# Performance work log

Measured on AMD Instinct MI355X. Metric: run time of the kernel, lower is better.

Reference implementation:

```python
import jax, jax.numpy as jnp
import numpy as np

N_NODES = 100000
N_EDGES = 1600000
D_IN = 128
D_OUT = 128
EPS = 1e-5


def setup_inputs() -> dict:
    key = jax.random.key(0)
    k1, k2, k3, k4, k5 = jax.random.split(key, 5)
    x = jax.random.normal(k1, (N_NODES, D_IN), dtype=jnp.float32)
    row = jax.random.randint(k2, (N_EDGES,), 0, N_NODES, dtype=jnp.int64)
    col = jax.random.randint(k3, (N_EDGES,), 0, N_NODES, dtype=jnp.int64)
    adj_vals = jax.random.uniform(k4, (N_EDGES,), dtype=jnp.float32)
    # Xavier-uniform init for weight, zeros for bias (as in the torch module)
    limit = float(np.sqrt(6.0 / (D_IN + D_OUT)))
    weight = jax.random.uniform(k5, (D_IN, D_OUT), minval=-limit, maxval=limit, dtype=jnp.float32)
    bias = jnp.zeros((D_OUT,), dtype=jnp.float32)
    return {"x": x, "row": row, "col": col, "adj_vals": adj_vals, "weight": weight, "bias": bias}


def reference(x, row, col, adj_vals, weight, bias):
    # degree = row-sum of sparse adj
    degree = jax.ops.segment_sum(adj_vals, row, num_segments=N_NODES)
    degree = jnp.where(degree == 0, EPS, degree)
    d_inv_sqrt = (degree + EPS) ** -0.5  # [N]
    # edge-wise symmetric normalization: D^-1/2 A D^-1/2
    edge_w = d_inv_sqrt[row] * adj_vals * d_inv_sqrt[col]  # [E]
    # SpMM: gather neighbor features, scale, scatter-add to destination rows
    msgs = edge_w[:, None] * x[col]  # [E, D_IN]
    agg = jax.ops.segment_sum(msgs, row, num_segments=N_NODES)  # [N, D_IN]
    return agg @ weight + bias
```

## Files before the change

### kernel.cpp

```cpp
#include <hip/hip_runtime.h>

#define NN 100000
#define NE 1600000
#define D  128
#define EPS 1e-5f

#define NBKT   782
#define NEB    391
#define EPB_H  4096
#define GRID_G 782
#define NSCAN  (NBKT*NEB)
#define GRID2  299
#define CAP    2560

#define OFF_HCNT 0x0000000ULL
#define OFF_PART 0x0140000ULL
#define OFF_BASE 0x0142000ULL
#define OFF_DINV 0x0150000ULL
#define OFF_GREC 0x0200000ULL
#define OFF_YB   0x0F00000ULL

typedef short short8 __attribute__((ext_vector_type(8)));
typedef float f32x4 __attribute__((ext_vector_type(4)));

static __device__ __forceinline__ unsigned f2bf(float f) {
    unsigned u = __float_as_uint(f);
    return (u + 0x7fffu + ((u >> 16) & 1u)) >> 16;
}

__global__ void k0h(const int* __restrict__ row, unsigned* __restrict__ hcnt) {
    __shared__ unsigned h[NBKT];
    int t = threadIdx.x, b = blockIdx.x;
    for (int i = t; i < NBKT; i += 256) h[i] = 0;
    __syncthreads();
    int ebeg = b * EPB_H;
    for (int i = t; i < EPB_H; i += 256) {
        int e = ebeg + i;
        if (e < NE) atomicAdd(&h[((unsigned)row[e]) >> 7], 1u);
    }
    __syncthreads();
    for (int i = t; i < NBKT; i += 256) hcnt[i * NEB + b] = h[i];
}

__global__ void k2a(const unsigned* __restrict__ hcnt, unsigned* __restrict__ part) {
    __shared__ unsigned s[256];
    int t = threadIdx.x;
    int gi = blockIdx.x * 1024 + t * 4;
    unsigned v = 0;
    #pragma unroll
    for (int j = 0; j < 4; ++j) if (gi + j < NSCAN) v += hcnt[gi + j];
    s[t] = v;
    __syncthreads();
    for (int d = 128; d > 0; d >>= 1) {
        if (t < d) s[t] += s[t + d];
        __syncthreads();
    }
    if (t == 0) part[blockIdx.x] = s[0];
}

__launch_bounds__(512)
__global__ void k2b(const unsigned* __restrict__ part, unsigned* __restrict__ base) {
    __shared__ unsigned s[512];
    int t = threadIdx.x;
    unsigned v = (t < GRID2) ? part[t] : 0;
    s[t] = v;
    __syncthreads();
    for (int d = 1; d < 512; d <<= 1) {
        unsigned u = (t >= d) ? s[t - d] : 0;
        __syncthreads();
        s[t] += u;
        __syncthreads();
    }
    if (t < GRID2) base[t] = s[t] - v;
}

__global__ void k2c(unsigned* __restrict__ hcnt, const unsigned* __restrict__ base) {
    __shared__ unsigned s[256];
    int t = threadIdx.x;
    int gi = blockIdx.x * 1024 + t * 4;
    unsigned v[4], tot = 0;
    #pragma unroll
    for (int j = 0; j < 4; ++j) {
        v[j] = (gi + j < NSCAN) ? hcnt[gi + j] : 0;
        tot += v[j];
    }
    s[t] = tot;
    __syncthreads();
    for (int d = 1; d < 256; d <<= 1) {
        unsigned u = (t >= d) ? s[t - d] : 0;
        __syncthreads();
        s[t] += u;
        __syncthreads();
    }
    unsigned run = base[blockIdx.x] + s[t] - tot;
    #pragma unroll
    for (int j = 0; j < 4; ++j) {
        if (gi + j < NSCAN) { hcnt[gi + j] = run; run += v[j]; }
    }
}

__launch_bounds__(256)
__global__ void k3(const int* __restrict__ row, const int* __restrict__ col,
                   const float* __restrict__ adj, const unsigned* __restrict__ hcnt,
                   unsigned long long* __restrict__ grec) {
    __shared__ unsigned cur[NBKT];
    int t = threadIdx.x, b = blockIdx.x;
    for (int i = t; i < NBKT; i += 256) cur[i] = hcnt[i * NEB + b];
    __syncthreads();
    int ebeg = b * EPB_H;
    for (int i = t; i < EPB_H; i += 256) {
        int e = ebeg + i;
        if (e >= NE) continue;
        unsigned r = (unsigned)row[e];
        unsigned aq = (unsigned)rintf(adj[e] * 32767.0f);
        unsigned lo = (unsigned)col[e] | (aq << 17);
        unsigned dst = atomicAdd(&cur[r >> 7], 1u);
        grec[dst] = (unsigned long long)lo | ((unsigned long long)(r & 127u) << 32);
    }
}

__global__ void k4a(const unsigned* __restrict__ hcnt, const unsigned long long* __restrict__ grec,
                    float* __restrict__ dinv) {
    __shared__ unsigned s[128];
    int t = threadIdx.x, b = blockIdx.x;
    if (t < 128) s[t] = 0;
    __syncthreads();
    unsigned beg = hcnt[b * NEB];
    unsigned end = (b == NBKT - 1) ? NE : hcnt[(b + 1) * NEB];
    for (unsigned p = beg + t; p < end; p += 256) {
        unsigned long long rec = grec[p];
        atomicAdd(&s[(unsigned)(rec >> 32) & 127u], ((unsigned)rec >> 17) & 0x7FFFu);
    }
    __syncthreads();
    if (t < 128) {
        int r = b * 128 + t;
        if (r < NN) {
            float d = (float)s[t] * (1.0f / 32767.0f);
            d = (d == 0.0f) ? EPS : d;
            dinv[r] = rsqrtf(d + EPS);
        }
    }
}

__launch_bounds__(256, 2)
__global__ void k1g(const float* __restrict__ x, const float* __restrict__ w,
                    const float* __restrict__ dinv, unsigned short* __restrict__ yb) {
    __shared__ unsigned short sx[128 * 128];
    __shared__ unsigned short sw[128 * 128];
    int tid = threadIdx.x;
    int base = blockIdx.x * 128;

    #pragma unroll
    for (int i = 0; i < 8; ++i) {
        int task = i * 256 + tid;
        int n = task & 127, ko = task >> 7;
        const float* wp = w + (size_t)(ko * 8) * D + n;
        uint4 pk;
        pk.x = f2bf(wp[0])     | (f2bf(wp[D])     << 16);
        pk.y = f2bf(wp[2 * D]) | (f2bf(wp[3 * D]) << 16);
        pk.z = f2bf(wp[4 * D]) | (f2bf(wp[5 * D]) << 16);
        pk.w = f2bf(wp[6 * D]) | (f2bf(wp[7 * D]) << 16);
        int idx = (n * 128 + ko * 8) ^ ((n & 7) << 3);
        *(uint4*)(&sw[idx]) = pk;
    }
    #pragma unroll
    for (int i = 0; i < 8; ++i) {
        int task = i * 256 + tid;
        int ko = task & 15, r = task >> 4;
        int gr = base + r;
        float4 f0 = make_float4(0.f, 0.f, 0.f, 0.f), f1 = f0;
        if (gr < NN) {
            const float* xp = x + (size_t)gr * D + ko * 8;
            f0 = *(const float4*)xp;
            f1 = *(const float4*)(xp + 4);
        }
        uint4 pk;
        pk.x = f2bf(f0.x) | (f2bf(f0.y) << 16);
        pk.y = f2bf(f0.z) | (f2bf(f0.w) << 16);
        pk.z = f2bf(f1.x) | (f2bf(f1.y) << 16);
        pk.w = f2bf(f1.z) | (f2bf(f1.w) << 16);
        int idx = (r * 128 + ko * 8) ^ ((r & 7) << 3);
        *(uint4*)(&sx[idx]) = pk;
    }
    __syncthreads();

    int wv = tid >> 6, l = tid & 63;
    int lr = l & 15, g = l >> 4;

    f32x4 acc[2][8];
    #pragma unroll
    for (int ti = 0; ti < 2; ++ti)
        #pragma unroll
        for (int tj = 0; tj < 8; ++tj)
            acc[ti][tj] = (f32x4){0.f, 0.f, 0.f, 0.f};

    #pragma unroll
    for (int kc = 0; kc < 4; ++kc) {
        int kb = kc * 32 + g * 8;
        short8 a[2], b[8];
        #pragma unroll
        for (int ti = 0; ti < 2; ++ti) {
            int r0 = wv * 32 + ti * 16 + lr;
            a[ti] = *(const short8*)(&sx[(r0 * 128 + kb) ^ ((r0 & 7) << 3)]);
        }
        #pragma unroll
        for (int tj = 0; tj < 8; ++tj) {
            int n0 = tj * 16 + lr;
            b[tj] = *(const short8*)(&sw[(n0 * 128 + kb) ^ ((n0 & 7) << 3)]);
        }
        #pragma unroll
        for (int ti = 0; ti < 2; ++ti)
            #pragma unroll
            for (int tj = 0; tj < 8; ++tj)
                acc[ti][tj] = __builtin_amdgcn_mfma_f32_16x16x32_bf16(
                    a[ti], b[tj], acc[ti][tj], 0, 0, 0);
    }

    #pragma unroll
    for (int ti = 0; ti < 2; ++ti) {
        #pragma unroll
        for (int reg = 0; reg < 4; ++reg) {
            int gr = base + wv * 32 + ti * 16 + g * 4 + reg;
            if (gr < NN) {
                float dv = dinv[gr];
                #pragma unroll
                for (int tj = 0; tj < 8; ++tj)
                    yb[(size_t)gr * D + tj * 16 + lr] =
                        (unsigned short)f2bf(acc[ti][tj][reg] * dv);
            }
        }
    }
}

__launch_bounds__(256, 4)
__global__ void k4b(const unsigned* __restrict__ hcnt, const unsigned long long* __restrict__ grec,
                    const float* __restrict__ dinv, const unsigned short* __restrict__ yb,
                    const float* __restrict__ bias, float* __restrict__ out) {
    __shared__ unsigned ecol[CAP + 8];
    __shared__ unsigned cnt[128], rb[128], cur[128], sc[128];
    int t = threadIdx.x, b = blockIdx.x;

    if (t < 128) cnt[t] = 0;
    __syncthreads();
    unsigned beg = hcnt[b * NEB];
    unsigned end = (b == NBKT - 1) ? NE : hcnt[(b + 1) * NEB];
    for (unsigned p = beg + t; p < end; p += 256)
        atomicAdd(&cnt[(unsigned)(grec[p] >> 32) & 127u], 1u);
    __syncthreads();

    if (t < 128) sc[t] = cnt[t];
    __syncthreads();
    for (int d = 1; d < 128; d <<= 1) {
        unsigned u = (t >= d && t < 128) ? sc[t - d] : 0;
        __syncthreads();
        if (t < 128) sc[t] += u;
        __syncthreads();
    }
    if (t < 128) { rb[t] = sc[t] - cnt[t]; cur[t] = sc[t] - cnt[t]; }
    __syncthreads();

    for (unsigned p = beg + t; p < end; p += 256) {
        unsigned long long rec = grec[p];
        unsigned rank = atomicAdd(&cur[(unsigned)(rec >> 32) & 127u], 1u);
        if (rank < CAP) ecol[rank] = (unsigned)rec;
    }
    __syncthreads();

    int grp = t >> 4, lq = t & 15;
    for (int k = 0; k < 8; ++k) {
        int rowlo = grp * 8 + k;
        int r = b * 128 + rowlo;
        if (r >= NN) continue;
        unsigned jb = rb[rowlo];
        unsigned c  = cnt[rowlo];
        unsigned jend = min(jb + c, (unsigned)CAP);

        float a0 = 0.f, a1 = 0.f, a2 = 0.f, a3 = 0.f;
        float a4 = 0.f, a5 = 0.f, a6 = 0.f, a7 = 0.f;

        for (unsigned j = jb; j < jend; j += 8) {
            unsigned ee[8];
            uint4 yq[8];
            float wv[8];
            int cm[8];
            #pragma unroll
            for (int u = 0; u < 8; ++u) ee[u] = ecol[j + u];
            #pragma unroll
            for (int u = 0; u < 8; ++u) cm[u] = min((int)(ee[u] & 0x1FFFFu), NN - 1);
            #pragma unroll
            for (int u = 0; u < 8; ++u)
                yq[u] = ((const uint4*)(yb + (size_t)cm[u] * D))[lq];
            #pragma unroll
            for (int u = 0; u < 8; ++u)
                wv[u] = (j + u < jend) ? (float)(ee[u] >> 17) : 0.f;
            #pragma unroll
            for (int u = 0; u < 8; ++u) {
                a0 += wv[u] * __uint_as_float(yq[u].x << 16);
                a1 += wv[u] * __uint_as_float(yq[u].x & 0xffff0000u);
                a2 += wv[u] * __uint_as_float(yq[u].y << 16);
                a3 += wv[u] * __uint_as_float(yq[u].y & 0xffff0000u);
                a4 += wv[u] * __uint_as_float(yq[u].z << 16);
                a5 += wv[u] * __uint_as_float(yq[u].z & 0xffff0000u);
                a6 += wv[u] * __uint_as_float(yq[u].w << 16);
                a7 += wv[u] * __uint_as_float(yq[u].w & 0xffff0000u);
            }
        }

        float scale = dinv[r] * (1.0f / 32767.0f);
        const float4* bp = (const float4*)bias + lq * 2;
        float4* op = (float4*)(out + (size_t)r * D) + lq * 2;
        float4 b0 = bp[0], b1 = bp[1];
        op[0] = make_float4(a0 * scale + b0.x, a1 * scale + b0.y,
                            a2 * scale + b0.z, a3 * scale + b0.w);
        op[1] = make_float4(a4 * scale + b1.x, a5 * scale + b1.y,
                            a6 * scale + b1.z, a7 * scale + b1.w);
    }
}

extern "C" void kernel_launch(void* const* d_in, const int* in_sizes, int n_in,
                              void* d_out, int out_size, void* d_ws, size_t ws_size,
                              hipStream_t stream) {
    const float* x    = (const float*)d_in[0];
    const int*   row  = (const int*)d_in[1];
    const int*   col  = (const int*)d_in[2];
    const float* adj  = (const float*)d_in[3];
    const float* wgt  = (const float*)d_in[4];
    const float* bias = (const float*)d_in[5];
    float* out = (float*)d_out;
    char*  ws  = (char*)d_ws;

    unsigned* hcnt  = (unsigned*)(ws + OFF_HCNT);
    unsigned* part  = (unsigned*)(ws + OFF_PART);
    unsigned* basep = (unsigned*)(ws + OFF_BASE);
    float*    dinv  = (float*)(ws + OFF_DINV);
    unsigned long long* grec = (unsigned long long*)(ws + OFF_GREC);
    unsigned short* yb = (unsigned short*)(ws + OFF_YB);

    k0h<<<NEB, 256, 0, stream>>>(row, hcnt);
    k2a<<<GRID2, 256, 0, stream>>>(hcnt, part);
    k2b<<<1, 512, 0, stream>>>(part, basep);
    k2c<<<GRID2, 256, 0, stream>>>(hcnt, basep);
    k3 <<<NEB, 256, 0, stream>>>(row, col, adj, hcnt, grec);
    k4a<<<NBKT, 256, 0, stream>>>(hcnt, grec, dinv);
    k1g<<<GRID_G, 256, 0, stream>>>(x, wgt, dinv, yb);
    k4b<<<NBKT, 256, 0, stream>>>(hcnt, grec, dinv, yb, bias, out);
}
```

Before: 144.4 us.

## Fold scan base pass into k2c, fuse degree into GEMM, unroll gather by 16

```diff
diff --git a/kernel.cpp b/kernel.cpp
--- a/kernel.cpp
+++ b/kernel.cpp
@@ -8,14 +8,12 @@
 #define NBKT   782
 #define NEB    391
 #define EPB_H  4096
-#define GRID_G 782
 #define NSCAN  (NBKT*NEB)
 #define GRID2  299
 #define CAP    2560
 
 #define OFF_HCNT 0x0000000ULL
 #define OFF_PART 0x0140000ULL
-#define OFF_BASE 0x0142000ULL
 #define OFF_DINV 0x0150000ULL
 #define OFF_GREC 0x0200000ULL
 #define OFF_YB   0x0F00000ULL
@@ -58,31 +56,30 @@
     if (t == 0) part[blockIdx.x] = s[0];
 }
 
-__launch_bounds__(512)
-__global__ void k2b(const unsigned* __restrict__ part, unsigned* __restrict__ base) {
-    __shared__ unsigned s[512];
-    int t = threadIdx.x;
-    unsigned v = (t < GRID2) ? part[t] : 0;
+__global__ void k2c(unsigned* __restrict__ hcnt, const unsigned* __restrict__ part) {
+    __shared__ unsigned s[256];
+    __shared__ unsigned bbase;
+    int t = threadIdx.x, g = blockIdx.x;
+
+    unsigned v = 0;
+    for (int i = t; i < g; i += 256) v += part[i];
     s[t] = v;
     __syncthreads();
-    for (int d = 1; d < 512; d <<= 1) {
-        unsigned u = (t >= d) ? s[t - d] : 0;
-        __syncthreads();
-        s[t] += u;
-        __syncthreads();
-    }
-    if (t < GRID2) base[t] = s[t] - v;
-}
-
-__global__ void k2c(unsigned* __restrict__ hcnt, const unsigned* __restrict__ base) {
-    __shared__ unsigned s[256];
-    int t = threadIdx.x;
-    int gi = blockIdx.x * 1024 + t * 4;
-    unsigned v[4], tot = 0;
+    for (int d = 128; d > 0; d >>= 1) {
+        if (t < d) s[t] += s[t + d];
+        __syncthreads();
+    }
+    if (t == 0) bbase = s[0];
+    __syncthreads();
+    unsigned base = bbase;
+    __syncthreads();
+
+    int gi = g * 1024 + t * 4;
+    unsigned w[4], tot = 0;
     #pragma unroll
     for (int j = 0; j < 4; ++j) {
-        v[j] = (gi + j < NSCAN) ? hcnt[gi + j] : 0;
-        tot += v[j];
+        w[j] = (gi + j < NSCAN) ? hcnt[gi + j] : 0;
+        tot += w[j];
     }
     s[t] = tot;
     __syncthreads();
@@ -92,10 +89,10 @@
         s[t] += u;
         __syncthreads();
     }
-    unsigned run = base[blockIdx.x] + s[t] - tot;
+    unsigned run = base + s[t] - tot;
     #pragma unroll
     for (int j = 0; j < 4; ++j) {
-        if (gi + j < NSCAN) { hcnt[gi + j] = run; run += v[j]; }
+        if (gi + j < NSCAN) { hcnt[gi + j] = run; run += w[j]; }
     }
 }
 
@@ -119,36 +116,36 @@
     }
 }
 
-__global__ void k4a(const unsigned* __restrict__ hcnt, const unsigned long long* __restrict__ grec,
-                    float* __restrict__ dinv) {
-    __shared__ unsigned s[128];
-    int t = threadIdx.x, b = blockIdx.x;
-    if (t < 128) s[t] = 0;
+__launch_bounds__(256, 2)
+__global__ void k1g(const float* __restrict__ x, const float* __restrict__ w,
+                    const unsigned* __restrict__ hcnt,
+                    const unsigned long long* __restrict__ grec,
+                    float* __restrict__ dinv_g, unsigned short* __restrict__ yb) {
+    __shared__ unsigned short sx[128 * 128];
+    __shared__ unsigned short sw[128 * 128];
+    __shared__ unsigned sdeg[128];
+    __shared__ float sdv[128];
+    int tid = threadIdx.x;
+    int b = blockIdx.x;
+    int base = b * 128;
+
+    if (tid < 128) sdeg[tid] = 0;
     __syncthreads();
     unsigned beg = hcnt[b * NEB];
     unsigned end = (b == NBKT - 1) ? NE : hcnt[(b + 1) * NEB];
-    for (unsigned p = beg + t; p < end; p += 256) {
+    for (unsigned p = beg + tid; p < end; p += 256) {
         unsigned long long rec = grec[p];
-        atomicAdd(&s[(unsigned)(rec >> 32) & 127u], ((unsigned)rec >> 17) & 0x7FFFu);
-    }
-    __syncthreads();
-    if (t < 128) {
-        int r = b * 128 + t;
-        if (r < NN) {
-            float d = (float)s[t] * (1.0f / 32767.0f);
-            d = (d == 0.0f) ? EPS : d;
-            dinv[r] = rsqrtf(d + EPS);
-        }
-    }
-}
-
-__launch_bounds__(256, 2)
-__global__ void k1g(const float* __restrict__ x, const float* __restrict__ w,
-                    const float* __restrict__ dinv, unsigned short* __restrict__ yb) {
-    __shared__ unsigned short sx[128 * 128];
-    __shared__ unsigned short sw[128 * 128];
-    int tid = threadIdx.x;
-    int base = blockIdx.x * 128;
+        atomicAdd(&sdeg[(unsigned)(rec >> 32) & 127u], ((unsigned)rec >> 17) & 0x7FFFu);
+    }
+    __syncthreads();
+    if (tid < 128) {
+        float d = (float)sdeg[tid] * (1.0f / 32767.0f);
+        d = (d == 0.0f) ? EPS : d;
+        float dv = rsqrtf(d + EPS);
+        sdv[tid] = dv;
+        int r = base + tid;
+        if (r < NN) dinv_g[r] = dv;
+    }
 
     #pragma unroll
     for (int i = 0; i < 8; ++i) {
@@ -197,7 +194,7 @@
     #pragma unroll
     for (int kc = 0; kc < 4; ++kc) {
         int kb = kc * 32 + g * 8;
-        short8 a[2], b[8];
+        short8 a[2], bb[8];
         #pragma unroll
         for (int ti = 0; ti < 2; ++ti) {
             int r0 = wv * 32 + ti * 16 + lr;
@@ -206,23 +203,24 @@
         #pragma unroll
         for (int tj = 0; tj < 8; ++tj) {
             int n0 = tj * 16 + lr;
-            b[tj] = *(const short8*)(&sw[(n0 * 128 + kb) ^ ((n0 & 7) << 3)]);
+            bb[tj] = *(const short8*)(&sw[(n0 * 128 + kb) ^ ((n0 & 7) << 3)]);
         }
         #pragma unroll
         for (int ti = 0; ti < 2; ++ti)
             #pragma unroll
             for (int tj = 0; tj < 8; ++tj)
                 acc[ti][tj] = __builtin_amdgcn_mfma_f32_16x16x32_bf16(
-                    a[ti], b[tj], acc[ti][tj], 0, 0, 0);
+                    a[ti], bb[tj], acc[ti][tj], 0, 0, 0);
     }
 
     #pragma unroll
     for (int ti = 0; ti < 2; ++ti) {
         #pragma unroll
         for (int reg = 0; reg < 4; ++reg) {
-            int gr = base + wv * 32 + ti * 16 + g * 4 + reg;
+            int lrow = wv * 32 + ti * 16 + g * 4 + reg;
+            int gr = base + lrow;
             if (gr < NN) {
-                float dv = dinv[gr];
+                float dv = sdv[lrow];
                 #pragma unroll
                 for (int tj = 0; tj < 8; ++tj)
                     yb[(size_t)gr * D + tj * 16 + lr] =
@@ -236,7 +234,7 @@
 __global__ void k4b(const unsigned* __restrict__ hcnt, const unsigned long long* __restrict__ grec,
                     const float* __restrict__ dinv, const unsigned short* __restrict__ yb,
                     const float* __restrict__ bias, float* __restrict__ out) {
-    __shared__ unsigned ecol[CAP + 8];
+    __shared__ unsigned ecol[CAP + 16];
     __shared__ unsigned cnt[128], rb[128], cur[128], sc[128];
     int t = threadIdx.x, b = blockIdx.x;
 
@@ -278,23 +276,23 @@
         float a0 = 0.f, a1 = 0.f, a2 = 0.f, a3 = 0.f;
         float a4 = 0.f, a5 = 0.f, a6 = 0.f, a7 = 0.f;
 
-        for (unsigned j = jb; j < jend; j += 8) {
-            unsigned ee[8];
-            uint4 yq[8];
-            float wv[8];
-            int cm[8];
-            #pragma unroll
-            for (int u = 0; u < 8; ++u) ee[u] = ecol[j + u];
-            #pragma unroll
-            for (int u = 0; u < 8; ++u) cm[u] = min((int)(ee[u] & 0x1FFFFu), NN - 1);
-            #pragma unroll
-            for (int u = 0; u < 8; ++u)
+        for (unsigned j = jb; j < jend; j += 16) {
+            unsigned ee[16];
+            uint4 yq[16];
+            float wv[16];
+            int cm[16];
+            #pragma unroll
+            for (int u = 0; u < 16; ++u) ee[u] = ecol[j + u];
+            #pragma unroll
+            for (int u = 0; u < 16; ++u) cm[u] = min((int)(ee[u] & 0x1FFFFu), NN - 1);
+            #pragma unroll
+            for (int u = 0; u < 16; ++u)
                 yq[u] = ((const uint4*)(yb + (size_t)cm[u] * D))[lq];
             #pragma unroll
-            for (int u = 0; u < 8; ++u)
+            for (int u = 0; u < 16; ++u)
                 wv[u] = (j + u < jend) ? (float)(ee[u] >> 17) : 0.f;
             #pragma unroll
-            for (int u = 0; u < 8; ++u) {
+            for (int u = 0; u < 16; ++u) {
                 a0 += wv[u] * __uint_as_float(yq[u].x << 16);
                 a1 += wv[u] * __uint_as_float(yq[u].x & 0xffff0000u);
                 a2 += wv[u] * __uint_as_float(yq[u].y << 16);
@@ -331,17 +329,14 @@
 
     unsigned* hcnt  = (unsigned*)(ws + OFF_HCNT);
     unsigned* part  = (unsigned*)(ws + OFF_PART);
-    unsigned* basep = (unsigned*)(ws + OFF_BASE);
     float*    dinv  = (float*)(ws + OFF_DINV);
     unsigned long long* grec = (unsigned long long*)(ws + OFF_GREC);
     unsigned short* yb = (unsigned short*)(ws + OFF_YB);
 
     k0h<<<NEB, 256, 0, stream>>>(row, hcnt);
     k2a<<<GRID2, 256, 0, stream>>>(hcnt, part);
-    k2b<<<1, 512, 0, stream>>>(part, basep);
-    k2c<<<GRID2, 256, 0, stream>>>(hcnt, basep);
+    k2c<<<GRID2, 256, 0, stream>>>(hcnt, part);
     k3 <<<NEB, 256, 0, stream>>>(row, col, adj, hcnt, grec);
-    k4a<<<NBKT, 256, 0, stream>>>(hcnt, grec, dinv);
-    k1g<<<GRID_G, 256, 0, stream>>>(x, wgt, dinv, yb);
+    k1g<<<NBKT, 256, 0, stream>>>(x, wgt, hcnt, grec, dinv, yb);
     k4b<<<NBKT, 256, 0, stream>>>(hcnt, grec, dinv, yb, bias, out);
 }
```

Result: slower. 147.5 us (+2.2%).
